# Optimization experiments

Measured on AMD Instinct MI355X. Metric: run time of the kernel, lower is better.

The kernel has to match this reference:

```python
import jax, jax.numpy as jnp
import numpy as np

N_NODES = 100000
D_IN = 128
H_DIM = 128
N_EDGES = 1600000


def _gcn_conv(x, src, dst, dinv, W, b):
    # PyG GCNConv(improved=True): h = x @ W; out = A_hat h + b,
    # A_hat = D^{-1/2} (A + 2I) D^{-1/2}
    h = x @ W                                   # [N, H]
    norm = dinv[src] * dinv[dst]                # [E]
    agg = jnp.zeros_like(h).at[dst].add(h[src] * norm[:, None])
    agg = agg + h * (2.0 * dinv * dinv)[:, None]  # self-loop, weight 2.0
    return agg + b


def setup_inputs() -> dict:
    key = jax.random.key(0)
    ks = jax.random.split(key, 12)
    s = 1.0 / np.sqrt(D_IN)
    sh = 1.0 / np.sqrt(2 * H_DIM)
    inp = {
        "x": jax.random.normal(ks[0], (N_NODES, D_IN), jnp.float32),
        "edge_index": jax.random.randint(ks[1], (2, N_EDGES), 0, N_NODES, jnp.int64),
        # GCNConv weights (in -> hidden), bias
        "Wz": jax.random.uniform(ks[2], (D_IN, H_DIM), jnp.float32, -s, s),
        "bz": jnp.zeros((H_DIM,), jnp.float32),
        "Wr": jax.random.uniform(ks[3], (D_IN, H_DIM), jnp.float32, -s, s),
        "br": jnp.zeros((H_DIM,), jnp.float32),
        "Wh": jax.random.uniform(ks[4], (D_IN, H_DIM), jnp.float32, -s, s),
        "bh": jnp.zeros((H_DIM,), jnp.float32),
        # TGCN gate linears: Linear(2h, h)
        "lzW": jax.random.uniform(ks[5], (2 * H_DIM, H_DIM), jnp.float32, -sh, sh),
        "lzb": jax.random.uniform(ks[6], (H_DIM,), jnp.float32, -sh, sh),
        "lrW": jax.random.uniform(ks[7], (2 * H_DIM, H_DIM), jnp.float32, -sh, sh),
        "lrb": jax.random.uniform(ks[8], (H_DIM,), jnp.float32, -sh, sh),
        "lhW": jax.random.uniform(ks[9], (2 * H_DIM, H_DIM), jnp.float32, -sh, sh),
        "lhb": jax.random.uniform(ks[10], (H_DIM,), jnp.float32, -sh, sh),
        # final linear2: hidden -> 1
        "W2": jax.random.uniform(ks[11], (H_DIM, 1), jnp.float32, -1 / np.sqrt(H_DIM), 1 / np.sqrt(H_DIM)),
        "b2": jnp.zeros((1,), jnp.float32),
    }
    return inp


def reference(x, edge_index, Wz, bz, Wr, br, Wh, bh, lzW, lzb, lrW, lrb, lhW, lhb, W2, b2):
    src, dst = edge_index[0], edge_index[1]
    n = x.shape[0]
    # improved GCN norm: deg includes self-loop weight 2
    deg = jnp.zeros((n,), x.dtype).at[dst].add(jnp.ones_like(src, x.dtype)) + 2.0
    dinv = jnp.where(deg > 0, deg ** -0.5, 0.0)
    # TGCN cell with H0 = 0
    H0 = jnp.zeros((n, Wz.shape[1]), x.dtype)
    Z = jax.nn.sigmoid(jnp.concatenate([_gcn_conv(x, src, dst, dinv, Wz, bz), H0], axis=1) @ lzW + lzb)
    R = jax.nn.sigmoid(jnp.concatenate([_gcn_conv(x, src, dst, dinv, Wr, br), H0], axis=1) @ lrW + lrb)
    Ht = jnp.tanh(jnp.concatenate([_gcn_conv(x, src, dst, dinv, Wh, bh), H0 * R], axis=1) @ lhW + lhb)
    H = Z * H0 + (1.0 - Z) * Ht
    # forward: relu output is discarded (y = h overwrites), then linear2
    return H @ W2 + b2
```

## Files before the change

kernel.cpp:

```cpp
#include <hip/hip_runtime.h>
#include <math.h>

#define D 128
#define BSHIFT 9
#define NB 196
#define EPT 7
#define P1B 241
#define CAPB 80
#define PSTRIDE (P1B * CAPB)
#define ECAP 9216
#define P2B NB
#define XCB2 3125
#define PRB 32

typedef __attribute__((ext_vector_type(8))) short s8v;
typedef __attribute__((ext_vector_type(8))) unsigned short us8;
typedef __attribute__((ext_vector_type(4))) unsigned short us4;
typedef __attribute__((ext_vector_type(4))) float f4v;

__device__ __forceinline__ float bf2f(unsigned short u) {
    union { unsigned int i; float f; } v; v.i = ((unsigned int)u) << 16; return v.f;
}
__device__ __forceinline__ unsigned short f2bf(float f) {
    union { float f; unsigned int i; } v; v.f = f;
    unsigned int r = v.i + 0x7FFFu + ((v.i >> 16) & 1u);
    return (unsigned short)(r >> 16);
}

__global__ __launch_bounds__(1024) void k_part1(
    const int* __restrict__ src, const int* __restrict__ dst, int E,
    unsigned int* __restrict__ pairs, int* __restrict__ runlen) {
    __shared__ int cnt[256];
    __shared__ int loff[256];
    __shared__ int ts[256];
    __shared__ unsigned int stage[EPT * 1024];
    int bx = blockIdx.x, tid = threadIdx.x;

    unsigned int pk[EPT]; int rkbk[EPT];
    int e0 = bx * (EPT * 1024) + tid;
    if (tid < 256) cnt[tid] = 0;
    __syncthreads();
    #pragma unroll
    for (int i = 0; i < EPT; ++i) {
        int e = e0 + i * 1024;
        bool ok = e < E;
        int d = ok ? dst[e] : 0;
        int s = ok ? src[e] : 0;
        int bk = d >> BSHIFT;
        pk[i] = ((unsigned int)(d & ((1 << BSHIFT) - 1)) << 17) | (unsigned int)s;
        int r = ok ? atomicAdd(&cnt[bk], 1) : 0;
        rkbk[i] = ok ? ((bk << 16) | r) : -1;
    }
    __syncthreads();
    if (tid < 256) ts[tid] = cnt[tid];
    __syncthreads();
    for (int off = 1; off < 256; off <<= 1) {
        int add = 0;
        if (tid < 256 && tid >= off) add = ts[tid - off];
        __syncthreads();
        if (tid < 256) ts[tid] += add;
        __syncthreads();
    }
    if (tid < 256) loff[tid] = ts[tid] - cnt[tid];
    __syncthreads();
    #pragma unroll
    for (int i = 0; i < EPT; ++i) {
        if (rkbk[i] >= 0) {
            int bk = rkbk[i] >> 16;
            stage[loff[bk] + (rkbk[i] & 0xffff)] = pk[i];
        }
    }
    if (tid < 256) runlen[bx * 256 + tid] = cnt[tid];
    __syncthreads();
    int wv = tid >> 6, lane = tid & 63;
    for (int b = wv; b < 256; b += 16) {
        int len = cnt[b];
        if (len == 0) continue;
        int lo = loff[b];
        unsigned int gbase = (unsigned int)b * PSTRIDE + (unsigned int)bx * CAPB;
        for (int j = lane; j < len; j += 64)
            pairs[gbase + j] = stage[lo + j];
    }
}

__global__ __launch_bounds__(1024) void k_mid(
    const unsigned int* __restrict__ pairs, const int* __restrict__ runlen,
    int N,
    int* __restrict__ rowptr, int* __restrict__ deg, float* __restrict__ dinv,
    int* __restrict__ esrc,
    const float* __restrict__ x, unsigned short* __restrict__ xb, int n4,
    const float* __restrict__ Wz, const float* __restrict__ bz,
    const float* __restrict__ lzW, const float* __restrict__ lzb,
    const float* __restrict__ Wh, const float* __restrict__ bh,
    const float* __restrict__ lhW, const float* __restrict__ lhb,
    unsigned short* __restrict__ Mt, float* __restrict__ c) {
    int bx = blockIdx.x, tid = threadIdx.x;

    if (bx < P2B) {
        __shared__ int cnt2[512];
        __shared__ int lcur[512];
        __shared__ int ts[256];
        __shared__ int rl[256];
        int b = bx;
        int n0 = b << BSHIFT;
        int nn = min(N - n0, 1 << BSHIFT);
        long pb = (long)b * PSTRIDE;
        int wv = tid >> 6, lane = tid & 63;

        if (tid < 256) rl[tid] = (tid < P1B) ? runlen[tid * 256 + b] : 0;
        if (tid < 512) cnt2[tid] = 0;
        __syncthreads();
        for (int r = wv; r < P1B; r += 16) {
            int len = rl[r];
            long rb = pb + r * CAPB;
            for (int j = lane; j < len; j += 64)
                atomicAdd(&cnt2[pairs[rb + j] >> 17], 1);
        }
        __syncthreads();
        int a0 = 0, a1 = 0, s = 0;
        if (tid < 256) {
            a0 = cnt2[2 * tid]; a1 = cnt2[2 * tid + 1];
            s = a0 + a1;
            ts[tid] = s;
        }
        __syncthreads();
        for (int off = 1; off < 256; off <<= 1) {
            int add = 0;
            if (tid < 256 && tid >= off) add = ts[tid - off];
            __syncthreads();
            if (tid < 256) ts[tid] += add;
            __syncthreads();
        }
        if (tid < 256) {
            int excl = ts[tid] - s;
            int base0 = b * ECAP + excl;
            lcur[2 * tid]     = base0;
            lcur[2 * tid + 1] = base0 + a0;
            if (2 * tid < nn) {
                rowptr[n0 + 2 * tid] = base0;
                deg[n0 + 2 * tid]    = a0;
                dinv[n0 + 2 * tid]   = rsqrtf((float)a0 + 2.0f);
            }
            if (2 * tid + 1 < nn) {
                rowptr[n0 + 2 * tid + 1] = base0 + a0;
                deg[n0 + 2 * tid + 1]    = a1;
                dinv[n0 + 2 * tid + 1]   = rsqrtf((float)a1 + 2.0f);
            }
        }
        __syncthreads();
        for (int r = wv; r < P1B; r += 16) {
            int len = rl[r];
            long rb = pb + r * CAPB;
            for (int j = lane; j < len; j += 64) {
                unsigned int p = pairs[rb + j];
                int dl = p >> 17;
                int pos = atomicAdd(&lcur[dl], 1);
                esrc[pos] = (int)(p & 0x1FFFFu);
            }
        }
    } else if (bx < P2B + XCB2) {
        int i = (bx - P2B) * 1024 + tid;
        if (i < n4) {
            float4 v = ((const float4*)x)[i];
            us4 o;
            o[0] = f2bf(v.x); o[1] = f2bf(v.y); o[2] = f2bf(v.z); o[3] = f2bf(v.w);
            ((us4*)xb)[i] = o;
        }
    } else {
        int k = (bx - (P2B + XCB2)) * 4 + (tid >> 8);
        int j = tid & 255;
        int jj = j & 127;
        const float* W = (j < 128) ? Wz : Wh;
        const float* L = (j < 128) ? lzW : lhW;
        float s = 0.f;
        for (int t = 0; t < 128; ++t) s += W[k * 128 + t] * L[t * 128 + jj];
        Mt[(size_t)j * 128 + k] = f2bf(s);
        if (k == 0) {
            const float* b  = (j < 128) ? bz  : bh;
            const float* lb = (j < 128) ? lzb : lhb;
            float cs = lb[jj];
            for (int t = 0; t < 128; ++t) cs += b[t] * L[t * 128 + jj];
            c[j] = cs;
        }
    }
}

__global__ __launch_bounds__(256) void k_gather(const unsigned short* __restrict__ xb,
                                                const int* __restrict__ esrc,
                                                const int* __restrict__ rowptr,
                                                const int* __restrict__ deg,
                                                const float* __restrict__ dinv,
                                                unsigned short* __restrict__ xab, int N) {
    int node = (blockIdx.x * blockDim.x + threadIdx.x) >> 5;
    int sub  = threadIdx.x & 31;
    if (node >= N) return;
    int eo = sub >> 4, cs = sub & 15;
    int start = rowptr[node];
    int end = start + deg[node];
    float dd = dinv[node];
    float acc[8];
    #pragma unroll
    for (int j = 0; j < 8; ++j) acc[j] = 0.f;

    for (int base = start; base < end; base += 32) {
        int cnt = min(32, end - base);
        int myedge = 0; float mynorm = 0.f;
        if (sub < cnt) { myedge = esrc[base + sub]; mynorm = dinv[myedge]; }
        int pairs = (cnt + 1) >> 1;
        int i = 0;
        for (; i + 3 < pairs; i += 4) {
            int i0 = 2 * i + eo;
            int   s0 = __shfl(myedge, i0,     32); float w0 = __shfl(mynorm, i0,     32);
            int   s1 = __shfl(myedge, i0 + 2, 32); float w1 = __shfl(mynorm, i0 + 2, 32);
            int   s2 = __shfl(myedge, i0 + 4, 32); float w2 = __shfl(mynorm, i0 + 4, 32);
            int   s3 = __shfl(myedge, i0 + 6, 32); float w3 = __shfl(mynorm, i0 + 6, 32);
            us8 v0 = *(const us8*)(xb + (size_t)s0 * D + cs * 8);
            us8 v1 = *(const us8*)(xb + (size_t)s1 * D + cs * 8);
            us8 v2 = *(const us8*)(xb + (size_t)s2 * D + cs * 8);
            us8 v3 = *(const us8*)(xb + (size_t)s3 * D + cs * 8);
            #pragma unroll
            for (int j = 0; j < 8; ++j) acc[j] += bf2f(v0[j]) * w0;
            #pragma unroll
            for (int j = 0; j < 8; ++j) acc[j] += bf2f(v1[j]) * w1;
            #pragma unroll
            for (int j = 0; j < 8; ++j) acc[j] += bf2f(v2[j]) * w2;
            #pragma unroll
            for (int j = 0; j < 8; ++j) acc[j] += bf2f(v3[j]) * w3;
        }
        for (; i < pairs; ++i) {
            int i0 = 2 * i + eo;
            int   s0 = __shfl(myedge, i0, 32); float w0 = __shfl(mynorm, i0, 32);
            us8 v0 = *(const us8*)(xb + (size_t)s0 * D + cs * 8);
            #pragma unroll
            for (int j = 0; j < 8; ++j) acc[j] += bf2f(v0[j]) * w0;
        }
    }
    #pragma unroll
    for (int j = 0; j < 8; ++j) acc[j] += __shfl_xor(acc[j], 16);
    if (eo == 0) {
        us8 xs = *(const us8*)(xb + (size_t)node * D + cs * 8);
        float sfac = 2.f * dd * dd;
        us8 r;
        #pragma unroll
        for (int j = 0; j < 8; ++j) r[j] = f2bf(acc[j] * dd + bf2f(xs[j]) * sfac);
        *(us8*)(xab + (size_t)node * D + cs * 8) = r;
    }
}

#define ASTRIDE 136
__global__ __launch_bounds__(256, 4) void k_ep_mfma(
    const unsigned short* __restrict__ xab, const unsigned short* __restrict__ Mt,
    const float* __restrict__ c, const float* __restrict__ W2,
    const float* __restrict__ b2, float* __restrict__ out, int N) {
    __shared__ unsigned short Ast[64 * ASTRIDE];
    __shared__ float pbuf[4][64];

    int tid = threadIdx.x;
    int n0 = blockIdx.x * 64;
    int wv = tid >> 6;
    int lane = tid & 63;
    int l = lane & 15, q = lane >> 4;

    #pragma unroll
    for (int j = 0; j < 4; ++j) {
        int idx = tid + 256 * j;
        int row = idx >> 4, c16 = idx & 15;
        us8 v = {0, 0, 0, 0, 0, 0, 0, 0};
        if (n0 + row < N) v = *(const us8*)(xab + (size_t)(n0 + row) * D + c16 * 8);
        *(us8*)&Ast[row * ASTRIDE + c16 * 8] = v;
    }
    __syncthreads();

    int tz0 = 2 * wv;
    f4v acc[4][4];
    #pragma unroll
    for (int i = 0; i < 4; ++i)
        #pragma unroll
        for (int nt = 0; nt < 4; ++nt) acc[i][nt] = (f4v){0.f, 0.f, 0.f, 0.f};

    const unsigned short* Bb = Mt + (size_t)l * 128 + q * 8;

    #pragma unroll
    for (int ks = 0; ks < 4; ++ks) {
        s8v b[4];
        #pragma unroll
        for (int i = 0; i < 2; ++i) {
            b[i]     = *(const s8v*)(Bb + (size_t)(tz0 + i) * 16 * 128 + ks * 32);
            b[2 + i] = *(const s8v*)(Bb + (size_t)(8 + tz0 + i) * 16 * 128 + ks * 32);
        }
        #pragma unroll
        for (int nt = 0; nt < 4; ++nt) {
            s8v a = *(const s8v*)&Ast[(nt * 16 + l) * ASTRIDE + ks * 32 + q * 8];
            #pragma unroll
            for (int i = 0; i < 4; ++i)
                acc[i][nt] = __builtin_amdgcn_mfma_f32_16x16x32_bf16(a, b[i], acc[i][nt], 0, 0, 0);
        }
    }

    float p[4][4];
    #pragma unroll
    for (int nt = 0; nt < 4; ++nt)
        #pragma unroll
        for (int r = 0; r < 4; ++r) p[nt][r] = 0.f;
    #pragma unroll
    for (int i = 0; i < 2; ++i) {
        int col = (tz0 + i) * 16 + l;
        float cz = c[col], ch = c[128 + col], w2 = W2[col];
        #pragma unroll
        for (int nt = 0; nt < 4; ++nt)
            #pragma unroll
            for (int r = 0; r < 4; ++r) {
                float gz = acc[i][nt][r] + cz;
                float gh = acc[2 + i][nt][r] + ch;
                float z  = 1.f / (1.f + __expf(-gz));
                float ht = 1.f - 2.f / (__expf(2.f * gh) + 1.f);
                p[nt][r] += (1.f - z) * ht * w2;
            }
    }
    #pragma unroll
    for (int nt = 0; nt < 4; ++nt)
        #pragma unroll
        for (int r = 0; r < 4; ++r) {
            p[nt][r] += __shfl_xor(p[nt][r], 1);
            p[nt][r] += __shfl_xor(p[nt][r], 2);
            p[nt][r] += __shfl_xor(p[nt][r], 4);
            p[nt][r] += __shfl_xor(p[nt][r], 8);
        }
    if (l == 0) {
        #pragma unroll
        for (int nt = 0; nt < 4; ++nt)
            #pragma unroll
            for (int r = 0; r < 4; ++r)
                pbuf[wv][nt * 16 + q * 4 + r] = p[nt][r];
    }
    __syncthreads();
    if (tid < 64) {
        int n = n0 + tid;
        if (n < N)
            out[n] = pbuf[0][tid] + pbuf[1][tid] + pbuf[2][tid] + pbuf[3][tid] + b2[0];
    }
}

extern "C" void kernel_launch(void* const* d_in, const int* in_sizes, int n_in,
                              void* d_out, int out_size, void* d_ws, size_t ws_size,
                              hipStream_t stream) {
    const float* x    = (const float*)d_in[0];
    const int*   eidx = (const int*)d_in[1];
    const float* Wz   = (const float*)d_in[2];
    const float* bz   = (const float*)d_in[3];
    const float* Wh   = (const float*)d_in[6];
    const float* bh   = (const float*)d_in[7];
    const float* lzW  = (const float*)d_in[8];
    const float* lzb  = (const float*)d_in[9];
    const float* lhW  = (const float*)d_in[12];
    const float* lhb  = (const float*)d_in[13];
    const float* W2   = (const float*)d_in[14];
    const float* b2   = (const float*)d_in[15];
    float* out = (float*)d_out;

    int N = in_sizes[0] / D;
    int E = in_sizes[1] / 2;
    const int* src = eidx;
    const int* dst = eidx + E;

    char* ws = (char*)d_ws;
    size_t off = 0;
    auto alloc = [&](size_t bytes) { void* p = ws + off; off += (bytes + 511) & ~(size_t)511; return p; };
    unsigned short* xb  = (unsigned short*)alloc((size_t)N * D * 2);
    unsigned short* xab = (unsigned short*)alloc((size_t)N * D * 2);
    int*   rowptr = (int*)  alloc((size_t)N * 4);
    int*   deg    = (int*)  alloc((size_t)N * 4);
    float* dinv   = (float*)alloc((size_t)N * 4);
    int*   esrc   = (int*)  alloc((size_t)NB * ECAP * 4);
    int*   runlen = (int*)  alloc((size_t)P1B * 256 * 4);
    unsigned short* Mt = (unsigned short*)alloc(256 * 128 * 2);
    float* c      = (float*)alloc(256 * 4);
    unsigned int* pairs = (unsigned int*)xab;

    int n4 = N * (D / 4);
    k_part1<<<P1B, 1024, 0, stream>>>(src, dst, E, pairs, runlen);
    k_mid<<<P2B + XCB2 + PRB, 1024, 0, stream>>>(
        pairs, runlen, N, rowptr, deg, dinv, esrc,
        x, xb, n4, Wz, bz, lzW, lzb, Wh, bh, lhW, lhb, Mt, c);
    k_gather<<<(N * 32 + 255) / 256, 256, 0, stream>>>(xb, esrc, rowptr, deg, dinv, xab, N);
    k_ep_mfma<<<(N + 63) / 64, 256, 0, stream>>>(xab, Mt, c, W2, b2, out, N);
}
```

Baseline: 239.5 us.

## Use wave-shuffle scans, LDS-staged CSR scatter, and deeper gather unrolling

The shared-memory Hillis-Steele prefix scans in the partition and mid kernels, which needed many block-wide barriers, become single-wavefront shuffle scans. The CSR fill in k_mid now scatters source indices into an LDS stage buffer and then writes them to global memory in one contiguous coalesced pass, instead of scattering straight to global. The gather kernel unrolls its edge loop to 8 outstanding row loads and issues the self-row load before the loop. The costs are more LDS per block in k_mid (a 36KB stage for every block, including the conversion and weight blocks), which can lower occupancy, and more registers in the gather kernel.

New measurement: 238.2 us. About the same (-0.5%).

```diff
diff --git a/kernel.cpp b/kernel.cpp
--- a/kernel.cpp
+++ b/kernel.cpp
@@ -32,7 +32,6 @@
     unsigned int* __restrict__ pairs, int* __restrict__ runlen) {
     __shared__ int cnt[256];
     __shared__ int loff[256];
-    __shared__ int ts[256];
     __shared__ unsigned int stage[EPT * 1024];
     int bx = blockIdx.x, tid = threadIdx.x;
 
@@ -52,16 +51,21 @@
         rkbk[i] = ok ? ((bk << 16) | r) : -1;
     }
     __syncthreads();
-    if (tid < 256) ts[tid] = cnt[tid];
-    __syncthreads();
-    for (int off = 1; off < 256; off <<= 1) {
-        int add = 0;
-        if (tid < 256 && tid >= off) add = ts[tid - off];
-        __syncthreads();
-        if (tid < 256) ts[tid] += add;
-        __syncthreads();
-    }
-    if (tid < 256) loff[tid] = ts[tid] - cnt[tid];
+    if (tid < 64) {
+        int v0 = cnt[tid * 4], v1 = cnt[tid * 4 + 1], v2 = cnt[tid * 4 + 2], v3 = cnt[tid * 4 + 3];
+        int s = v0 + v1 + v2 + v3;
+        int sc = s;
+        #pragma unroll
+        for (int off = 1; off < 64; off <<= 1) {
+            int o = __shfl_up(sc, off, 64);
+            if (tid >= off) sc += o;
+        }
+        int excl = sc - s;
+        loff[tid * 4]     = excl;
+        loff[tid * 4 + 1] = excl + v0;
+        loff[tid * 4 + 2] = excl + v0 + v1;
+        loff[tid * 4 + 3] = excl + v0 + v1 + v2;
+    }
     __syncthreads();
     #pragma unroll
     for (int i = 0; i < EPT; ++i) {
@@ -94,13 +98,14 @@
     const float* __restrict__ Wh, const float* __restrict__ bh,
     const float* __restrict__ lhW, const float* __restrict__ lhb,
     unsigned short* __restrict__ Mt, float* __restrict__ c) {
+    __shared__ int cnt2[512];
+    __shared__ int lcur[512];
+    __shared__ int rl[256];
+    __shared__ int sstage[ECAP];
+    __shared__ int stot;
     int bx = blockIdx.x, tid = threadIdx.x;
 
     if (bx < P2B) {
-        __shared__ int cnt2[512];
-        __shared__ int lcur[512];
-        __shared__ int ts[256];
-        __shared__ int rl[256];
         int b = bx;
         int n0 = b << BSHIFT;
         int nn = min(N - n0, 1 << BSHIFT);
@@ -117,34 +122,28 @@
                 atomicAdd(&cnt2[pairs[rb + j] >> 17], 1);
         }
         __syncthreads();
-        int a0 = 0, a1 = 0, s = 0;
-        if (tid < 256) {
-            a0 = cnt2[2 * tid]; a1 = cnt2[2 * tid + 1];
-            s = a0 + a1;
-            ts[tid] = s;
-        }
-        __syncthreads();
-        for (int off = 1; off < 256; off <<= 1) {
-            int add = 0;
-            if (tid < 256 && tid >= off) add = ts[tid - off];
-            __syncthreads();
-            if (tid < 256) ts[tid] += add;
-            __syncthreads();
-        }
-        if (tid < 256) {
-            int excl = ts[tid] - s;
-            int base0 = b * ECAP + excl;
-            lcur[2 * tid]     = base0;
-            lcur[2 * tid + 1] = base0 + a0;
-            if (2 * tid < nn) {
-                rowptr[n0 + 2 * tid] = base0;
-                deg[n0 + 2 * tid]    = a0;
-                dinv[n0 + 2 * tid]   = rsqrtf((float)a0 + 2.0f);
-            }
-            if (2 * tid + 1 < nn) {
-                rowptr[n0 + 2 * tid + 1] = base0 + a0;
-                deg[n0 + 2 * tid + 1]    = a1;
-                dinv[n0 + 2 * tid + 1]   = rsqrtf((float)a1 + 2.0f);
+        if (tid < 64) {
+            int v[8]; int s = 0;
+            #pragma unroll
+            for (int k = 0; k < 8; ++k) { v[k] = cnt2[tid * 8 + k]; s += v[k]; }
+            int sc = s;
+            #pragma unroll
+            for (int off = 1; off < 64; off <<= 1) {
+                int o = __shfl_up(sc, off, 64);
+                if (tid >= off) sc += o;
+            }
+            int excl = sc - s;
+            if (tid == 63) stot = sc;
+            #pragma unroll
+            for (int k = 0; k < 8; ++k) {
+                int node = tid * 8 + k;
+                lcur[node] = excl;
+                if (node < nn) {
+                    rowptr[n0 + node] = b * ECAP + excl;
+                    deg[n0 + node]    = v[k];
+                    dinv[n0 + node]   = rsqrtf((float)v[k] + 2.0f);
+                }
+                excl += v[k];
             }
         }
         __syncthreads();
@@ -153,11 +152,14 @@
             long rb = pb + r * CAPB;
             for (int j = lane; j < len; j += 64) {
                 unsigned int p = pairs[rb + j];
-                int dl = p >> 17;
-                int pos = atomicAdd(&lcur[dl], 1);
-                esrc[pos] = (int)(p & 0x1FFFFu);
-            }
-        }
+                int pos = atomicAdd(&lcur[p >> 17], 1);
+                sstage[pos] = (int)(p & 0x1FFFFu);
+            }
+        }
+        __syncthreads();
+        int tot = stot;
+        for (int i = tid; i < tot; i += 1024)
+            esrc[b * ECAP + i] = sstage[i];
     } else if (bx < P2B + XCB2) {
         int i = (bx - P2B) * 1024 + tid;
         if (i < n4) {
@@ -198,6 +200,8 @@
     int start = rowptr[node];
     int end = start + deg[node];
     float dd = dinv[node];
+    us8 xs = {0, 0, 0, 0, 0, 0, 0, 0};
+    if (eo == 0) xs = *(const us8*)(xb + (size_t)node * D + cs * 8);
     float acc[8];
     #pragma unroll
     for (int j = 0; j < 8; ++j) acc[j] = 0.f;
@@ -206,9 +210,27 @@
         int cnt = min(32, end - base);
         int myedge = 0; float mynorm = 0.f;
         if (sub < cnt) { myedge = esrc[base + sub]; mynorm = dinv[myedge]; }
-        int pairs = (cnt + 1) >> 1;
+        int npairs = (cnt + 1) >> 1;
         int i = 0;
-        for (; i + 3 < pairs; i += 4) {
+        for (; i + 7 < npairs; i += 8) {
+            int i0 = 2 * i + eo;
+            int se[8]; float we[8];
+            #pragma unroll
+            for (int u = 0; u < 8; ++u) {
+                se[u] = __shfl(myedge, i0 + 2 * u, 32);
+                we[u] = __shfl(mynorm, i0 + 2 * u, 32);
+            }
+            us8 v[8];
+            #pragma unroll
+            for (int u = 0; u < 8; ++u)
+                v[u] = *(const us8*)(xb + (size_t)se[u] * D + cs * 8);
+            #pragma unroll
+            for (int u = 0; u < 8; ++u) {
+                #pragma unroll
+                for (int j = 0; j < 8; ++j) acc[j] += bf2f(v[u][j]) * we[u];
+            }
+        }
+        for (; i + 3 < npairs; i += 4) {
             int i0 = 2 * i + eo;
             int   s0 = __shfl(myedge, i0,     32); float w0 = __shfl(mynorm, i0,     32);
             int   s1 = __shfl(myedge, i0 + 2, 32); float w1 = __shfl(mynorm, i0 + 2, 32);
@@ -227,7 +249,7 @@
             #pragma unroll
             for (int j = 0; j < 8; ++j) acc[j] += bf2f(v3[j]) * w3;
         }
-        for (; i < pairs; ++i) {
+        for (; i < npairs; ++i) {
             int i0 = 2 * i + eo;
             int   s0 = __shfl(myedge, i0, 32); float w0 = __shfl(mynorm, i0, 32);
             us8 v0 = *(const us8*)(xb + (size_t)s0 * D + cs * 8);
@@ -238,7 +260,6 @@
     #pragma unroll
     for (int j = 0; j < 8; ++j) acc[j] += __shfl_xor(acc[j], 16);
     if (eo == 0) {
-        us8 xs = *(const us8*)(xb + (size_t)node * D + cs * 8);
         float sfac = 2.f * dd * dd;
         us8 r;
         #pragma unroll
```
